# Optimization experiments

Hardware: AMD Instinct MI355X
Metric: run time of the kernel (lower is better)

The kernel has to match this reference:

```python
import jax, jax.numpy as jnp
import numpy as np

NUM_HEADS = 16
STRIDE = 32
WINDOW = 64  # local window half-width hard-coded in the original forward


def setup_inputs() -> dict:
    key = jax.random.key(0)
    k0, k1, k2 = jax.random.split(key, 3)
    d = 1024
    return {
        "x": jax.random.normal(k0, (1, 2048, d), dtype=jnp.float32),
        "w_qkv": jax.random.normal(k1, (d, 3 * d), dtype=jnp.float32) / np.sqrt(d),
        "b_qkv": jnp.zeros((3 * d,), dtype=jnp.float32),
        "w_out": jax.random.normal(k2, (d, d), dtype=jnp.float32) / np.sqrt(d),
        "b_out": jnp.zeros((d,), dtype=jnp.float32),
    }


def _sparse_mask(n: int) -> jnp.ndarray:
    # mask[i, j] True if j is a strided column (j % stride == 0)
    # or j is within the +/-WINDOW local band of i.
    i = jnp.arange(n)[:, None]
    j = jnp.arange(n)[None, :]
    return (j % STRIDE == 0) | (jnp.abs(i - j) <= WINDOW)


def reference(x, w_qkv, b_qkv, w_out, b_out):
    b, n, d = x.shape
    h = NUM_HEADS
    dh = d // h
    scale = dh ** (-0.5)

    qkv = x @ w_qkv + b_qkv  # [b, n, 3d]
    q, k, v = jnp.split(qkv, 3, axis=-1)
    q = q.reshape(b, n, h, dh).transpose(0, 2, 1, 3)  # [b, h, n, dh]
    k = k.reshape(b, n, h, dh).transpose(0, 2, 1, 3)
    v = v.reshape(b, n, h, dh).transpose(0, 2, 1, 3)

    scores = jnp.einsum("bhid,bhjd->bhij", q, k) * scale  # [b, h, n, n]
    mask = _sparse_mask(n)  # [n, n], broadcast over b, h
    scores = jnp.where(mask, scores, -jnp.inf)
    attn = jax.nn.softmax(scores, axis=-1)

    out = jnp.einsum("bhij,bhjd->bhid", attn, v)  # [b, h, n, dh]
    out = out.transpose(0, 2, 1, 3).reshape(b, n, d)
    return out @ w_out + b_out
```

## Files before the change

kernel.cpp:

```cpp
#include <hip/hip_runtime.h>

typedef unsigned short u16;
typedef __attribute__((ext_vector_type(8))) short bf16x8;
typedef __attribute__((ext_vector_type(4))) float f32x4;

__device__ __forceinline__ u16 f2bf(float f) {
  union { float f; unsigned u; } v; v.f = f;
  unsigned u = v.u;
  return (u16)((u + 0x7FFFu + ((u >> 16) & 1u)) >> 16);
}

__device__ __forceinline__ void gld16(const void* g, void* l) {
  __builtin_amdgcn_global_load_lds((const __attribute__((address_space(1))) void*)g,
                                   (__attribute__((address_space(3))) void*)l, 16, 0, 0);
}

__device__ __forceinline__ void tconv64(const float* __restrict__ in, u16* __restrict__ out,
                                        int R, int C, int bc, int br, float* t) {
  const int tid = threadIdx.x;
  const int c0 = bc * 64, r0 = br * 64;
  const int hi = tid >> 4, lo = tid & 15;
#pragma unroll
  for (int it = 0; it < 4; ++it) {
    int r = it * 16 + hi;
    float4 f = *(const float4*)&in[(size_t)(r0 + r) * C + c0 + lo * 4];
    float* tr = &t[r * 65 + lo * 4];
    tr[0] = f.x; tr[1] = f.y; tr[2] = f.z; tr[3] = f.w;
  }
  __syncthreads();
#pragma unroll
  for (int it = 0; it < 4; ++it) {
    int cc = it * 16 + hi;
    ushort4 o;
    o.x = f2bf(t[(lo * 4 + 0) * 65 + cc]);
    o.y = f2bf(t[(lo * 4 + 1) * 65 + cc]);
    o.z = f2bf(t[(lo * 4 + 2) * 65 + cc]);
    o.w = f2bf(t[(lo * 4 + 3) * 65 + cc]);
    *(ushort4*)&out[(size_t)(c0 + cc) * R + r0 + lo * 4] = o;
  }
}

__global__ __launch_bounds__(256) void prep(const float* __restrict__ x, u16* __restrict__ xb,
                                            const float* __restrict__ wq, u16* __restrict__ wqT,
                                            const float* __restrict__ wo, u16* __restrict__ woT) {
  __shared__ float t[64 * 65];
  int b = blockIdx.x;
  if (b < 1024) {
    int i = (b * 256 + threadIdx.x) * 8;
    float4 f0 = *(const float4*)(x + i);
    float4 f1 = *(const float4*)(x + i + 4);
    ushort4 r0, r1;
    r0.x = f2bf(f0.x); r0.y = f2bf(f0.y); r0.z = f2bf(f0.z); r0.w = f2bf(f0.w);
    r1.x = f2bf(f1.x); r1.y = f2bf(f1.y); r1.z = f2bf(f1.z); r1.w = f2bf(f1.w);
    *(ushort4*)(xb + i) = r0;
    *(ushort4*)(xb + i + 4) = r1;
  } else if (b < 1024 + 768) {
    int b2 = b - 1024;
    tconv64(wq, wqT, 1024, 3072, b2 % 48, b2 / 48, t);
  } else {
    int b3 = b - 1792;
    tconv64(wo, woT, 1024, 1024, b3 & 15, b3 >> 4, t);
  }
}

#define GEMM_STAGE(As, Bs, A, BT, buf, kt, BM, BN, MT, NT)                        \
  {                                                                               \
    _Pragma("unroll")                                                             \
    for (int it = 0; it < MT; ++it) {                                             \
      int G = wv * (MT * 64) + it * 64 + lane;                                    \
      int r = G >> 3, g = G & 7, gs = g ^ (r & 7);                                \
      gld16(&A[(size_t)(m0 + r) * K + (kt) + gs * 8],                             \
            &As[buf][(wv * (MT * 64) + it * 64) * 8]);                            \
    }                                                                             \
    _Pragma("unroll")                                                             \
    for (int it = 0; it < NT; ++it) {                                             \
      int G = wv * (NT * 64) + it * 64 + lane;                                    \
      int r = G >> 3, g = G & 7, gs = g ^ (r & 7);                                \
      gld16(&BT[(size_t)(n0 + r) * K + (kt) + gs * 8],                            \
            &Bs[buf][(wv * (NT * 64) + it * 64) * 8]);                            \
    }                                                                             \
  }

#define GEMM_COMPUTE(As, Bs, buf, BM, BN, MT, NT)                                 \
  {                                                                               \
    _Pragma("unroll")                                                             \
    for (int ks = 0; ks < 2; ++ks) {                                              \
      bf16x8 av[MT], bv[NT];                                                      \
      _Pragma("unroll")                                                           \
      for (int m = 0; m < MT; ++m) {                                              \
        int r = wm * (BM / 2) + m * 16 + lr;                                      \
        av[m] = *(const bf16x8*)&As[buf][r * 64 + (((ks * 4 + lg) ^ (r & 7)) * 8)]; \
      }                                                                           \
      _Pragma("unroll")                                                           \
      for (int n = 0; n < NT; ++n) {                                              \
        int r = wn * (BN / 2) + n * 16 + lr;                                      \
        bv[n] = *(const bf16x8*)&Bs[buf][r * 64 + (((ks * 4 + lg) ^ (r & 7)) * 8)]; \
      }                                                                           \
      _Pragma("unroll")                                                           \
      for (int m = 0; m < MT; ++m)                                                \
        _Pragma("unroll")                                                         \
        for (int n = 0; n < NT; ++n)                                              \
          acc[m][n] = __builtin_amdgcn_mfma_f32_16x16x32_bf16(av[m], bv[n],       \
                                                              acc[m][n], 0, 0, 0); \
    }                                                                             \
  }

__global__ __launch_bounds__(256) void gemm_qkv(const u16* __restrict__ A,
                                                const u16* __restrict__ BT,
                                                const float* __restrict__ bias,
                                                u16* __restrict__ qkv3,
                                                u16* __restrict__ vT,
                                                u16* __restrict__ vTs,
                                                int K) {
  constexpr int BM = 128, BN = 64, MT = 4, NT = 2;
  __shared__ u16 As[2][BM * 64];
  __shared__ u16 Bs[2][BN * 64];
  const int tid = threadIdx.x;
  const int lane = tid & 63, wv = tid >> 6;
  const int lr = lane & 15, lg = lane >> 4;
  const int wm = wv >> 1, wn = wv & 1;
  const int m0 = blockIdx.y * BM, n0 = blockIdx.x * BN;

  f32x4 acc[MT][NT] = {};

  GEMM_STAGE(As, Bs, A, BT, 0, 0, BM, BN, MT, NT);
  __syncthreads();
  int cur = 0;
  for (int kt = 64; kt < K; kt += 64) {
    GEMM_STAGE(As, Bs, A, BT, cur ^ 1, kt, BM, BN, MT, NT);
    GEMM_COMPUTE(As, Bs, cur, BM, BN, MT, NT);
    __syncthreads();
    cur ^= 1;
  }
  GEMM_COMPUTE(As, Bs, cur, BM, BN, MT, NT);

  if (n0 < 2048) {
#pragma unroll
    for (int m = 0; m < MT; ++m)
#pragma unroll
      for (int n = 0; n < NT; ++n) {
        int col = n0 + wn * 32 + n * 16 + lr;
        float bcol = bias[col];
#pragma unroll
        for (int qq = 0; qq < 4; ++qq) {
          int row = m0 + wm * 64 + m * 16 + 4 * lg + qq;
          qkv3[(size_t)row * 3072 + col] = f2bf(acc[m][n][qq] + bcol);
        }
      }
  } else {
    __syncthreads();
    u16* T = &As[0][0];
#pragma unroll
    for (int m = 0; m < MT; ++m)
#pragma unroll
      for (int n = 0; n < NT; ++n) {
        int col = wn * 32 + n * 16 + lr;
        float bcol = bias[n0 + col];
#pragma unroll
        for (int qq = 0; qq < 4; ++qq) {
          int row = wm * 64 + m * 16 + 4 * lg + qq;
          T[col * 132 + row] = f2bf(acc[m][n][qq] + bcol);
        }
      }
    __syncthreads();
    const int dgb = n0 - 2048;
#pragma unroll
    for (int c = wv; c < 64; c += 4) {
      uint val = (uint)T[c * 132 + lane * 2] | ((uint)T[c * 132 + lane * 2 + 1] << 16);
      *(uint*)&vT[(size_t)(dgb + c) * 2048 + m0 + lane * 2] = val;
    }
    {
      int rr = tid >> 6, c = tid & 63;
      vTs[(size_t)(dgb + c) * 64 + (m0 >> 5) + rr] = T[c * 132 + rr * 32];
    }
  }
}

__global__ __launch_bounds__(256) void gemm_out(const u16* __restrict__ A,
                                                const u16* __restrict__ BT,
                                                const float* __restrict__ bias,
                                                float* __restrict__ Cp,
                                                int K) {
  constexpr int BM = 64, BN = 64, MT = 2, NT = 2;
  __shared__ u16 As[2][BM * 64];
  __shared__ u16 Bs[2][BN * 64];
  const int tid = threadIdx.x;
  const int lane = tid & 63, wv = tid >> 6;
  const int lr = lane & 15, lg = lane >> 4;
  const int wm = wv >> 1, wn = wv & 1;
  const int m0 = blockIdx.y * BM, n0 = blockIdx.x * BN;

  f32x4 acc[MT][NT] = {};

  GEMM_STAGE(As, Bs, A, BT, 0, 0, BM, BN, MT, NT);
  __syncthreads();
  int cur = 0;
  for (int kt = 64; kt < K; kt += 64) {
    GEMM_STAGE(As, Bs, A, BT, cur ^ 1, kt, BM, BN, MT, NT);
    GEMM_COMPUTE(As, Bs, cur, BM, BN, MT, NT);
    __syncthreads();
    cur ^= 1;
  }
  GEMM_COMPUTE(As, Bs, cur, BM, BN, MT, NT);

#pragma unroll
  for (int m = 0; m < MT; ++m)
#pragma unroll
    for (int n = 0; n < NT; ++n) {
      int col = n0 + wn * 32 + n * 16 + lr;
      float bcol = bias[col];
#pragma unroll
      for (int qq = 0; qq < 4; ++qq) {
        int row = m0 + wm * 32 + m * 16 + 4 * lg + qq;
        Cp[(size_t)row * 1024 + col] = acc[m][n][qq] + bcol;
      }
    }
}

__global__ __launch_bounds__(256) void sattn(const u16* __restrict__ qkv,
                                             const u16* __restrict__ vT,
                                             const u16* __restrict__ vTs,
                                             u16* __restrict__ ao) {
  const int h = blockIdx.x;
  const int i0b = blockIdx.y * 64;
  const int ws = i0b - 64;
  const int tid = threadIdx.x;
  const int lane = tid & 63, wv = tid >> 6;
  const int lr = lane & 15, lg = lane >> 4;

  __shared__ __attribute__((aligned(16))) u16 Kl[256 * 64];
  __shared__ __attribute__((aligned(16))) u16 Vl[64 * 256];
  __shared__ __attribute__((aligned(16))) u16 Ps[4][16][264];

#pragma unroll
  for (int it = 0; it < 8; ++it) {
    {
      int ck = wv * 8 + it;
      int c = 8 * ck + (lane >> 3);
      int g = lane & 7, gs = g ^ (c & 7);
      int j = (c < 192) ? (ws + c) : ((c - 192) << 5);
      j = j < 0 ? 0 : (j > 2047 ? 2047 : j);
      gld16(&qkv[(size_t)j * 3072 + 1024 + h * 64 + gs * 8], &Kl[ck * 512]);
    }
    {
      int tv = wv * 8 + it;
      int d = 2 * tv + (lane >> 5);
      int g = lane & 31, gs = g ^ (d & 7);
      const u16* src;
      if (gs < 24) {
        int c0 = ws + gs * 8;
        c0 = c0 < 0 ? 0 : (c0 > 2040 ? 2040 : c0);
        src = &vT[(size_t)(h * 64 + d) * 2048 + c0];
      } else {
        src = &vTs[(size_t)(h * 64 + d) * 64 + (gs - 24) * 8];
      }
      gld16(src, &Vl[tv * 512]);
    }
  }
  __syncthreads();

  const int i0 = i0b + wv * 16;
  const u16* qp = &qkv[(size_t)(i0 + lr) * 3072 + h * 64 + lg * 8];
  bf16x8 qa0 = *(const bf16x8*)qp;
  bf16x8 qa1 = *(const bf16x8*)(qp + 32);

  f32x4 sc[16];
#pragma unroll
  for (int n = 0; n < 16; ++n) {
    int c = n * 16 + lr;
    bf16x8 k0 = *(const bf16x8*)&Kl[c * 64 + ((lg ^ (c & 7)) * 8)];
    bf16x8 k1 = *(const bf16x8*)&Kl[c * 64 + (((4 + lg) ^ (c & 7)) * 8)];
    f32x4 a = {0.f, 0.f, 0.f, 0.f};
    a = __builtin_amdgcn_mfma_f32_16x16x32_bf16(qa0, k0, a, 0, 0, 0);
    a = __builtin_amdgcn_mfma_f32_16x16x32_bf16(qa1, k1, a, 0, 0, 0);
    sc[n] = a;
  }

  float mx[4] = {-1e30f, -1e30f, -1e30f, -1e30f};
#pragma unroll
  for (int n = 0; n < 16; ++n) {
    int c = n * 16 + lr;
    int jw = ws + c;
    int js = (c - 192) << 5;
    bool isw = c < 192;
#pragma unroll
    for (int qq = 0; qq < 4; ++qq) {
      int i = i0 + 4 * lg + qq;
      bool ok;
      if (isw) {
        int dd = i - jw; dd = dd < 0 ? -dd : dd;
        ok = (jw >= 0) && (jw < 2048) && ((dd <= 64) || ((jw & 31) == 0));
      } else {
        ok = (js < ws) || (js >= ws + 192);
      }
      float v = ok ? sc[n][qq] * 0.125f : -1e30f;
      sc[n][qq] = v;
      mx[qq] = fmaxf(mx[qq], v);
    }
  }
#pragma unroll
  for (int qq = 0; qq < 4; ++qq) {
    float v = mx[qq];
    v = fmaxf(v, __shfl_xor(v, 1));
    v = fmaxf(v, __shfl_xor(v, 2));
    v = fmaxf(v, __shfl_xor(v, 4));
    v = fmaxf(v, __shfl_xor(v, 8));
    mx[qq] = v;
  }

  float sm[4] = {0.f, 0.f, 0.f, 0.f};
#pragma unroll
  for (int n = 0; n < 16; ++n) {
#pragma unroll
    for (int qq = 0; qq < 4; ++qq) {
      float p = __expf(sc[n][qq] - mx[qq]);
      sm[qq] += p;
      Ps[wv][4 * lg + qq][n * 16 + lr] = f2bf(p);
    }
  }
#pragma unroll
  for (int qq = 0; qq < 4; ++qq) {
    float s = sm[qq];
    s += __shfl_xor(s, 1);
    s += __shfl_xor(s, 2);
    s += __shfl_xor(s, 4);
    s += __shfl_xor(s, 8);
    sm[qq] = s;
  }
  __syncthreads();

  f32x4 ov[4] = {{0.f,0.f,0.f,0.f},{0.f,0.f,0.f,0.f},{0.f,0.f,0.f,0.f},{0.f,0.f,0.f,0.f}};
#pragma unroll
  for (int ksb = 0; ksb < 8; ++ksb) {
    bf16x8 pa = *(const bf16x8*)&Ps[wv][lr][ksb * 32 + lg * 8];
#pragma unroll
    for (int n = 0; n < 4; ++n) {
      int d = n * 16 + lr;
      bf16x8 vb = *(const bf16x8*)&Vl[d * 256 + (((ksb * 4 + lg) ^ (d & 7)) * 8)];
      ov[n] = __builtin_amdgcn_mfma_f32_16x16x32_bf16(pa, vb, ov[n], 0, 0, 0);
    }
  }

#pragma unroll
  for (int qq = 0; qq < 4; ++qq) {
    float inv = 1.0f / sm[qq];
    int row = i0 + 4 * lg + qq;
#pragma unroll
    for (int n = 0; n < 4; ++n)
      ao[(size_t)row * 1024 + h * 64 + n * 16 + lr] = f2bf(ov[n][qq] * inv);
  }
}

extern "C" void kernel_launch(void* const* d_in, const int* in_sizes, int n_in,
                              void* d_out, int out_size, void* d_ws, size_t ws_size,
                              hipStream_t stream) {
  (void)in_sizes; (void)n_in; (void)out_size; (void)ws_size;
  const float* x     = (const float*)d_in[0];
  const float* w_qkv = (const float*)d_in[1];
  const float* b_qkv = (const float*)d_in[2];
  const float* w_out = (const float*)d_in[3];
  const float* b_out = (const float*)d_in[4];
  float* out = (float*)d_out;
  char* ws = (char*)d_ws;

  u16* xb    = (u16*)(ws);
  u16* wqkvT = (u16*)(ws + 4194304);
  u16* woutT = (u16*)(ws + 10485760);
  u16* qkv3  = (u16*)(ws + 12582912);
  u16* attnb = (u16*)(ws + 25165824);
  u16* vT    = (u16*)(ws + 29360128);
  u16* vTs   = (u16*)(ws + 33554432);

  prep<<<2048, 256, 0, stream>>>(x, xb, w_qkv, wqkvT, w_out, woutT);
  gemm_qkv<<<dim3(3072 / 64, 2048 / 128), 256, 0, stream>>>(xb, wqkvT, b_qkv, qkv3, vT, vTs,
                                                            1024);
  sattn<<<dim3(16, 32), 256, 0, stream>>>(qkv3, vT, vTs, attnb);
  gemm_out<<<dim3(1024 / 64, 2048 / 64), 256, 0, stream>>>(attnb, woutT, b_out, out, 1024);
}
```

Baseline: 59.51 us.

## Widen QKV GEMM tiles to 96 columns and remap blocks XCD-aware

The QKV GEMM tile grows from 128x64 to 128x96, giving 512 blocks, and the epilogue now handles tiles that straddle the K/V boundary by writing partial columns to both qkv3 and the transposed V buffers. All three main kernels switch to a 1D grid of 512 blocks with a remap (orig&7)*64 + orig>>3. The remap is meant to place neighbouring tiles on the same XCD for better L2 reuse, and the grid now matches a CU-count multiple. The cost is a more complex epilogue with data-dependent loops and higher register use from NT=3.

New measurement: 63.12 us. 1.06x slower.

```diff
diff --git a/kernel.cpp b/kernel.cpp
--- a/kernel.cpp
+++ b/kernel.cpp
@@ -112,14 +112,16 @@
                                                 u16* __restrict__ vT,
                                                 u16* __restrict__ vTs,
                                                 int K) {
-  constexpr int BM = 128, BN = 64, MT = 4, NT = 2;
+  constexpr int BM = 128, BN = 96, MT = 4, NT = 3;
   __shared__ u16 As[2][BM * 64];
   __shared__ u16 Bs[2][BN * 64];
   const int tid = threadIdx.x;
   const int lane = tid & 63, wv = tid >> 6;
   const int lr = lane & 15, lg = lane >> 4;
   const int wm = wv >> 1, wn = wv & 1;
-  const int m0 = blockIdx.y * BM, n0 = blockIdx.x * BN;
+  const int orig = blockIdx.x;
+  const int wg = (orig & 7) * 64 + (orig >> 3);
+  const int n0 = (wg & 31) * 96, m0 = (wg >> 5) * 128;
 
   f32x4 acc[MT][NT] = {};
 
@@ -139,7 +141,7 @@
     for (int m = 0; m < MT; ++m)
 #pragma unroll
       for (int n = 0; n < NT; ++n) {
-        int col = n0 + wn * 32 + n * 16 + lr;
+        int col = n0 + wn * 48 + n * 16 + lr;
         float bcol = bias[col];
 #pragma unroll
         for (int qq = 0; qq < 4; ++qq) {
@@ -147,31 +149,36 @@
           qkv3[(size_t)row * 3072 + col] = f2bf(acc[m][n][qq] + bcol);
         }
       }
-  } else {
+  }
+  int cl0 = (n0 >= 2048) ? 0 : (n0 + 96 <= 2048 ? 96 : 2048 - n0);
+  if (cl0 < 96) {
     __syncthreads();
     u16* T = &As[0][0];
 #pragma unroll
     for (int m = 0; m < MT; ++m)
 #pragma unroll
       for (int n = 0; n < NT; ++n) {
-        int col = wn * 32 + n * 16 + lr;
-        float bcol = bias[n0 + col];
-#pragma unroll
-        for (int qq = 0; qq < 4; ++qq) {
-          int row = wm * 64 + m * 16 + 4 * lg + qq;
-          T[col * 132 + row] = f2bf(acc[m][n][qq] + bcol);
+        int cb = wn * 48 + n * 16;
+        if (cb >= cl0) {
+          int col = cb + lr;
+          float bcol = bias[n0 + col];
+#pragma unroll
+          for (int qq = 0; qq < 4; ++qq) {
+            int row = wm * 64 + m * 16 + 4 * lg + qq;
+            T[col * 132 + row] = f2bf(acc[m][n][qq] + bcol);
+          }
         }
       }
     __syncthreads();
-    const int dgb = n0 - 2048;
-#pragma unroll
-    for (int c = wv; c < 64; c += 4) {
+    for (int c = cl0 + wv; c < 96; c += 4) {
+      int dg = n0 - 2048 + c;
       uint val = (uint)T[c * 132 + lane * 2] | ((uint)T[c * 132 + lane * 2 + 1] << 16);
-      *(uint*)&vT[(size_t)(dgb + c) * 2048 + m0 + lane * 2] = val;
-    }
-    {
-      int rr = tid >> 6, c = tid & 63;
-      vTs[(size_t)(dgb + c) * 64 + (m0 >> 5) + rr] = T[c * 132 + rr * 32];
+      *(uint*)&vT[(size_t)dg * 2048 + m0 + lane * 2] = val;
+    }
+    int ncols = 96 - cl0;
+    for (int u = tid; u < 4 * ncols; u += 256) {
+      int rr = u / ncols, c = cl0 + (u - rr * ncols);
+      vTs[(size_t)(n0 - 2048 + c) * 64 + (m0 >> 5) + rr] = T[c * 132 + rr * 32];
     }
   }
 }
@@ -188,7 +195,9 @@
   const int lane = tid & 63, wv = tid >> 6;
   const int lr = lane & 15, lg = lane >> 4;
   const int wm = wv >> 1, wn = wv & 1;
-  const int m0 = blockIdx.y * BM, n0 = blockIdx.x * BN;
+  const int orig = blockIdx.x;
+  const int wg = (orig & 7) * 64 + (orig >> 3);
+  const int n0 = (wg & 15) * 64, m0 = (wg >> 4) * 64;
 
   f32x4 acc[MT][NT] = {};
 
@@ -221,8 +230,10 @@
                                              const u16* __restrict__ vT,
                                              const u16* __restrict__ vTs,
                                              u16* __restrict__ ao) {
-  const int h = blockIdx.x;
-  const int i0b = blockIdx.y * 64;
+  const int orig = blockIdx.x;
+  const int wg = (orig & 7) * 64 + (orig >> 3);
+  const int h = wg >> 5;
+  const int i0b = (wg & 31) * 64;
   const int ws = i0b - 64;
   const int tid = threadIdx.x;
   const int lane = tid & 63, wv = tid >> 6;
@@ -372,8 +383,7 @@
   u16* vTs   = (u16*)(ws + 33554432);
 
   prep<<<2048, 256, 0, stream>>>(x, xb, w_qkv, wqkvT, w_out, woutT);
-  gemm_qkv<<<dim3(3072 / 64, 2048 / 128), 256, 0, stream>>>(xb, wqkvT, b_qkv, qkv3, vT, vTs,
-                                                            1024);
-  sattn<<<dim3(16, 32), 256, 0, stream>>>(qkv3, vT, vTs, attnb);
-  gemm_out<<<dim3(1024 / 64, 2048 / 64), 256, 0, stream>>>(attnb, woutT, b_out, out, 1024);
-}
+  gemm_qkv<<<512, 256, 0, stream>>>(xb, wqkvT, b_qkv, qkv3, vT, vTs, 1024);
+  sattn<<<512, 256, 0, stream>>>(qkv3, vT, vTs, attnb);
+  gemm_out<<<512, 256, 0, stream>>>(attnb, woutT, b_out, out, 1024);
+}
```
